# Kernel optimization log

Measured on AMD Instinct MI355X. Metric: run time of the kernel, lower is better.

## Reference

```python
import jax, jax.numpy as jnp
import numpy as np

N, B, D_IN, UNITS, K = 8192, 1, 2, 64, 2
F = D_IN + UNITS        # concatenated feature size per node
M = K + 1               # number of diffusion matrices (x0..xK)


def setup_inputs() -> dict:
    key = jax.random.key(0)
    k1, k2, k3, k4, k5, k6 = jax.random.split(key, 6)
    inputs = jax.random.normal(k1, (B, N * D_IN), dtype=jnp.float32)
    hx = jax.random.normal(k2, (B, N * UNITS), dtype=jnp.float32)
    adj = jax.random.uniform(k3, (N, N), dtype=jnp.float32)
    w_ru = jax.random.normal(k4, (F * M, 2 * UNITS), dtype=jnp.float32) * (2.0 / (F * M + 2 * UNITS)) ** 0.5
    b_ru = jnp.ones((2 * UNITS,), dtype=jnp.float32)  # bias_start=1.0 for gates
    w_c = jax.random.normal(k5, (F * M, UNITS), dtype=jnp.float32) * (2.0 / (F * M + UNITS)) ** 0.5
    b_c = jnp.zeros((UNITS,), dtype=jnp.float32)
    node_index = jax.random.randint(k6, (N,), 0, N)
    return {"inputs": inputs, "hx": hx, "adj": adj, "w_ru": w_ru,
            "b_ru": b_ru, "w_c": w_c, "b_c": b_c, "node_index": node_index}


def _gconv(adj_mx, inp, state, W, b, out_size):
    # inp: [B, N, D_IN], state: [B, N, UNITS]
    x = jnp.concatenate([inp, state], axis=2)              # [B, N, F]
    x0 = jnp.transpose(x, (1, 2, 0)).reshape(N, F * B)     # [N, F*B]
    xs = [x0]
    x1 = adj_mx @ x0                                       # 1-hop diffusion
    xs.append(x1)
    for _ in range(2, K + 1):                              # Chebyshev-style recurrence
        x2 = 2.0 * (adj_mx @ x1) - x0
        xs.append(x2)
        x0, x1 = x1, x2
    xk = jnp.stack(xs, 0).reshape(M, N, F, B)              # [M, N, F, B]
    xk = jnp.transpose(xk, (3, 1, 2, 0)).reshape(B * N, F * M)
    out = xk @ W + b                                       # [B*N, out_size]
    return out.reshape(B, N * out_size)


def reference(inputs, hx, adj, w_ru, b_ru, w_c, b_c, node_index):
    # square adj branch: adj_mx = ((D^-1)(A+I))^T, d_mat_inv = I (unused)
    adj2 = adj + jnp.eye(N, dtype=adj.dtype)
    d_inv = 1.0 / jnp.sum(adj2, axis=1)                    # no inf: diagonal added
    adj_mx = (adj2 * d_inv[:, None]).T
    inp = inputs.reshape(B, N, D_IN)
    h3 = hx.reshape(B, N, UNITS)
    value = jax.nn.sigmoid(_gconv(adj_mx, inp, h3, w_ru, b_ru, 2 * UNITS))
    value = value.reshape(B, N, 2 * UNITS)
    r = value[..., :UNITS].reshape(B, N * UNITS)
    u = value[..., UNITS:].reshape(B, N * UNITS)
    c = jnp.tanh(_gconv(adj_mx, inp, (r * hx).reshape(B, N, UNITS), w_c, b_c, UNITS))
    new_state = u * hx + (1.0 - u) * c                     # [B, N*UNITS]
    return new_state
```

## Files before the change

### kernel.cpp

```cpp
#include <hip/hip_runtime.h>
#include <math.h>


typedef __attribute__((ext_vector_type(4))) float f32x4;
typedef __attribute__((ext_vector_type(2))) int v2i;
typedef __attribute__((ext_vector_type(4))) int v4i;
typedef unsigned char uch;

constexpr int NN  = 8192;
constexpr int CST = 80;
constexpr int KBT = 256;
constexpr int SFT = KBT / 2;
constexpr int MCH = 4;
constexpr size_t NS    = (size_t)NN * CST;
constexpr size_t UTFS8 = (size_t)SFT * 5 * 1024;

constexpr float SC1  = 4096.f,   ISC1 = 1.f / 4096.f;
constexpr float SC2  = 262144.f, ISC2 = 1.f / 262144.f;

static __device__ __forceinline__ unsigned f2e4m3(float x) {
  union { float f; unsigned u; } c; c.f = x;
  unsigned s = (c.u >> 24) & 0x80u;
  float a = fabsf(x);
  if (a >= 464.f) return s | 0x7Eu;
  if (a < 0.015625f) {
    int q = (int)(a * 512.f + 0.5f);
    return s | (unsigned)q;
  }
  c.f = a;
  unsigned u = c.u + (0x7FFFFu + ((c.u >> 20) & 1u));
  int e = (int)((u >> 23) & 0xFFu) - 127;
  unsigned m = (u >> 20) & 7u;
  if (e > 8) return s | 0x7Eu;
  return s | (unsigned)(((e + 7) << 3) | m);
}

static __device__ __forceinline__ void mfma_f8(f32x4& acc, v2i a, v2i b) {
  asm("v_mfma_f32_16x16x32_fp8_fp8 %0, %1, %2, %0" : "+v"(acc) : "v"(a), "v"(b));
}
static __device__ __forceinline__ v2i lo2(v4i v) { v2i r; r.x = v.x; r.y = v.y; return r; }
static __device__ __forceinline__ v2i hi2(v4i v) { v2i r; r.x = v.z; r.y = v.w; return r; }

__global__ __launch_bounds__(256, 4) void k_conv(const float* __restrict__ adj,
                                                 uch* __restrict__ adjF8,
                                                 float* __restrict__ dpart) {
  __shared__ float tile[2][32][132];
  const int kb = blockIdx.x, mc = blockIdx.y;
  const int tid = threadIdx.x;
  const int l = tid & 63, w = tid >> 6;
  const int rg = tid >> 5;
  const int cb = (tid & 31) * 4;
  const float* src = adj + ((size_t)kb * 32 + rg) * NN + (size_t)mc * 2048 + cb;
  float rs[4] = {0.f, 0.f, 0.f, 0.f};
  float4 vA[4], vB[4];

#pragma unroll
  for (int i = 0; i < 4; ++i)
    vA[i] = *(const float4*)(src + (size_t)(8 * i) * NN);

#define CONV_BODY(CH, BUF, VC, VN)                                             \
  {                                                                            \
    const int ch_ = (CH);                                                      \
    _Pragma("unroll") for (int i = 0; i < 4; ++i) {                            \
      int r = rg + 8 * i;                                                      \
      int colp = (cb + 8 * i) & 127;                                           \
      *(float4*)&tile[BUF][r][colp] = VC[i];                                   \
      rs[i] += (VC[i].x + VC[i].y) + (VC[i].z + VC[i].w);                      \
    }                                                                          \
    if (ch_ < 15) {                                                            \
      _Pragma("unroll") for (int i = 0; i < 4; ++i)                            \
          VN[i] = *(const float4*)(src + (size_t)(8 * i) * NN + (ch_ + 1) * 128); \
    }                                                                          \
    __syncthreads();                                                           \
    _Pragma("unroll") for (int h = 0; h < 2; ++h) {                            \
      int fl = w + 4 * h;                                                      \
      int mt = mc * 128 + ch_ * 8 + fl;                                        \
      int colp = (fl * 16 + (l & 15) + 8 * (l >> 4)) & 127;                    \
      unsigned plo = 0, phi = 0;                                               \
      _Pragma("unroll") for (int j = 0; j < 4; ++j)                            \
        plo |= f2e4m3(tile[BUF][8 * (l >> 4) + j][colp]) << (8 * j);           \
      _Pragma("unroll") for (int j = 4; j < 8; ++j)                            \
        phi |= f2e4m3(tile[BUF][8 * (l >> 4) + j][colp]) << (8 * (j - 4));     \
      uint2 pk; pk.x = plo; pk.y = phi;                                        \
      *(uint2*)(adjF8 + ((size_t)mt * SFT + (kb >> 1)) * 1024                  \
                + l * 16 + (kb & 1) * 8) = pk;                                 \
    }                                                                          \
  }

  for (int cp = 0; cp < 8; ++cp) {
    CONV_BODY(2 * cp,     0, vA, vB);
    CONV_BODY(2 * cp + 1, 1, vB, vA);
  }
#undef CONV_BODY

#pragma unroll
  for (int i = 0; i < 4; ++i) {
#pragma unroll
    for (int m = 16; m >= 1; m >>= 1) rs[i] += __shfl_xor(rs[i], m);
  }
  if ((tid & 31) == 0) {
#pragma unroll
    for (int i = 0; i < 4; ++i)
      dpart[(size_t)mc * NN + kb * 32 + 8 * i + rg] = rs[i];
  }
}

__global__ __launch_bounds__(256) void k_build(const float* __restrict__ hx,
                                               const float* __restrict__ inp,
                                               const float* __restrict__ dpart,
                                               float* __restrict__ dinv,
                                               float* __restrict__ X0,
                                               float* __restrict__ XS0,
                                               uch* __restrict__ UtF8) {
  __shared__ float dv_s[32];
  const int bid = blockIdx.x;
  const int n0 = bid * 32;
  const int tid = threadIdx.x;
  if (tid < 32) {
    int n = n0 + tid;
    float dv = 1.f / (dpart[n] + dpart[NN + n] + dpart[2 * NN + n] +
                      dpart[3 * NN + n] + 1.f);
    dv_s[tid] = dv;
    dinv[n] = dv;
  }
  __syncthreads();
  for (int p = tid; p < 32 * 20; p += 256) {
    int nl = p / 20, c4 = (p % 20) * 4;
    int n = n0 + nl;
    float dv = dv_s[nl];
    float v[4];
#pragma unroll
    for (int j = 0; j < 4; ++j) {
      int c = c4 + j;
      v[j] = (c < 64) ? hx[n * 64 + c] : (c < 66 ? inp[n * 2 + (c - 64)] : 0.f);
    }
    size_t o = (size_t)n * CST + c4;
    *(float4*)(X0 + o)  = make_float4(v[0], v[1], v[2], v[3]);
    *(float4*)(XS0 + o) = make_float4(dv * v[0], dv * v[1], dv * v[2], dv * v[3]);
  }
  for (int p = tid; p < 5 * 64; p += 256) {
    int nt = p >> 6, l = p & 63;
    unsigned plo = 0, phi = 0;
#pragma unroll
    for (int j = 0; j < 8; ++j) {
      int nloc = 8 * (l >> 4) + j;
      int n = n0 + nloc;
      int c = nt * 16 + (l & 15);
      float v = (c < 64) ? hx[n * 64 + c] : (c < 66 ? inp[n * 2 + (c - 64)] : 0.f);
      unsigned b = f2e4m3(v * dv_s[nloc] * SC1);
      if (j < 4) plo |= b << (8 * j); else phi |= b << (8 * (j - 4));
    }
    uint2 pk; pk.x = plo; pk.y = phi;
    *(uint2*)(UtF8 + ((size_t)(bid >> 1) * 5 + nt) * 1024 + l * 16 + (bid & 1) * 8) = pk;
  }
}

static __device__ __forceinline__ void gemm_core2(const uch* __restrict__ adjF8,
                                                  const uch* __restrict__ bF8,
                                                  int bid, int tid, float* smem,
                                                  float sv[5], float inv_scale) {
  const int w8 = tid >> 6, l = tid & 63;
  const int sf0 = w8 * 16;
  f32x4 acc0[5], acc1[5];
#pragma unroll
  for (int nt = 0; nt < 5; ++nt) {
    acc0[nt] = (f32x4){0.f, 0.f, 0.f, 0.f};
    acc1[nt] = (f32x4){0.f, 0.f, 0.f, 0.f};
  }
  const uch* ap = adjF8 + ((size_t)(2 * bid) * SFT + sf0) * 1024 + l * 16;
  const size_t MSTR = (size_t)SFT * 1024;
  const uch* bp = bF8 + (size_t)sf0 * 5 * 1024 + l * 16;

  v4i A0e, A1e, A0o, A1o, Be[5], Bo[5];
  A0e = *(const v4i*)(ap);
  A1e = *(const v4i*)(ap + MSTR);
#pragma unroll
  for (int nt = 0; nt < 5; ++nt) Be[nt] = *(const v4i*)(bp + nt * 1024);

  for (int sf = 0; sf < 16; sf += 2) {
    A0o = *(const v4i*)(ap + (size_t)(sf + 1) * 1024);
    A1o = *(const v4i*)(ap + MSTR + (size_t)(sf + 1) * 1024);
#pragma unroll
    for (int nt = 0; nt < 5; ++nt)
      Bo[nt] = *(const v4i*)(bp + (size_t)((sf + 1) * 5 + nt) * 1024);
#pragma unroll
    for (int nt = 0; nt < 5; ++nt) {
      mfma_f8(acc0[nt], lo2(A0e), lo2(Be[nt]));
      mfma_f8(acc1[nt], lo2(A1e), lo2(Be[nt]));
    }
#pragma unroll
    for (int nt = 0; nt < 5; ++nt) {
      mfma_f8(acc0[nt], hi2(A0e), hi2(Be[nt]));
      mfma_f8(acc1[nt], hi2(A1e), hi2(Be[nt]));
    }
    A0e = *(const v4i*)(ap + (size_t)(sf + 2) * 1024);
    A1e = *(const v4i*)(ap + MSTR + (size_t)(sf + 2) * 1024);
#pragma unroll
    for (int nt = 0; nt < 5; ++nt)
      Be[nt] = *(const v4i*)(bp + (size_t)((sf + 2) * 5 + nt) * 1024);
#pragma unroll
    for (int nt = 0; nt < 5; ++nt) {
      mfma_f8(acc0[nt], lo2(A0o), lo2(Bo[nt]));
      mfma_f8(acc1[nt], lo2(A1o), lo2(Bo[nt]));
    }
#pragma unroll
    for (int nt = 0; nt < 5; ++nt) {
      mfma_f8(acc0[nt], hi2(A0o), hi2(Bo[nt]));
      mfma_f8(acc1[nt], hi2(A1o), hi2(Bo[nt]));
    }
  }
  asm volatile("s_nop 7\n\ts_nop 7\n\ts_nop 7" ::: "memory");

  auto red = reinterpret_cast<float(*)[64][40]>(smem);
  if (w8 < 4) {
#pragma unroll
    for (int nt = 0; nt < 5; ++nt) {
      *(f32x4*)&red[w8][l][nt * 4]      = acc0[nt];
      *(f32x4*)&red[w8][l][20 + nt * 4] = acc1[nt];
    }
  }
  __syncthreads();
  if (w8 >= 4) {
#pragma unroll
    for (int nt = 0; nt < 5; ++nt) {
      f32x4 t0 = *(f32x4*)&red[w8 - 4][l][nt * 4];
      f32x4 t1 = *(f32x4*)&red[w8 - 4][l][20 + nt * 4];
      *(f32x4*)&red[w8 - 4][l][nt * 4]      = t0 + acc0[nt];
      *(f32x4*)&red[w8 - 4][l][20 + nt * 4] = t1 + acc1[nt];
    }
  }
  __syncthreads();
#pragma unroll
  for (int i = 0; i < 5; ++i) {
    int p = tid + i * 512;
    int r = p / 80, c = p % 80;
    int mtl = r >> 4, rl = r & 15;
    int ll = ((rl >> 2) << 4) | (c & 15);
    int slot = mtl * 20 + (((c >> 4) << 2) | (rl & 3));
    sv[i] = (((red[0][ll][slot] + red[1][ll][slot]) +
              red[2][ll][slot]) + red[3][ll][slot]) * inv_scale;
  }
  __syncthreads();
}

__global__ __launch_bounds__(512, 1) void k_hop1(const uch* __restrict__ adjF8,
                                                 const uch* __restrict__ UtFin,
                                                 const float* __restrict__ XSin,
                                                 const float* __restrict__ dinv,
                                                 float* __restrict__ X1,
                                                 float* __restrict__ XS1,
                                                 uch* __restrict__ UtFout) {
  __shared__ __align__(16) float smem[10240];
  const int bid = blockIdx.x, tid = threadIdx.x;
  const int n0 = bid * 32;
  float sv[5];
  gemm_core2(adjF8, UtFin, bid, tid, smem, sv, ISC1);

  auto xs = reinterpret_cast<float(*)[80]>(smem);
#pragma unroll
  for (int i = 0; i < 5; ++i) {
    int p = tid + i * 512;
    size_t o = (size_t)n0 * CST + p;
    float x1 = XSin[o] + sv[i];
    X1[o] = x1;
    float z = dinv[n0 + p / 80] * x1;
    XS1[o] = z;
    xs[p / 80][p % 80] = z;
  }
  __syncthreads();
  for (int p = tid; p < 5 * 64; p += 512) {
    int nt = p >> 6, l = p & 63;
    unsigned plo = 0, phi = 0;
#pragma unroll
    for (int j = 0; j < 8; ++j) {
      unsigned b = f2e4m3(xs[8 * (l >> 4) + j][nt * 16 + (l & 15)] * SC2);
      if (j < 4) plo |= b << (8 * j); else phi |= b << (8 * (j - 4));
    }
    uint2 pk; pk.x = plo; pk.y = phi;
    *(uint2*)(UtFout + ((size_t)(bid >> 1) * 5 + nt) * 1024 + l * 16 + (bid & 1) * 8) = pk;
  }
}

__global__ __launch_bounds__(512, 1) void k_hop2g(const uch* __restrict__ adjF8,
    const uch* __restrict__ UtFb, const float* __restrict__ XS1,
    const float* __restrict__ X0, const float* __restrict__ X1,
    const float* __restrict__ w_ru, const float* __restrict__ b_ru,
    const float* __restrict__ hx, const float* __restrict__ inp,
    const float* __restrict__ dinv,
    float* __restrict__ X0w, float* __restrict__ XS0w,
    uch* __restrict__ UtFa, float* __restrict__ UG) {
  __shared__ __align__(16) float smem[10240];
  const int bid = blockIdx.x, tid = threadIdx.x;
  const int n0 = bid * 32;
  float sv[5];
  gemm_core2(adjF8, UtFb, bid, tid, smem, sv, ISC2);

  auto xr2 = reinterpret_cast<float(*)[80]>(smem);
  float* xr01 = smem + 2560;
  float* rhq  = smem + 2560 + 4352;
#pragma unroll
  for (int i = 0; i < 5; ++i) {
    int p = tid + i * 512;
    size_t o = (size_t)n0 * CST + p;
    xr2[p / 80][p % 80] = 2.f * (XS1[o] + sv[i]) - X0[o];
  }
  for (int p = tid; p < 32 * 17; p += 512) {
    int nl = p / 17, c4 = (p % 17) * 4;
    size_t o = (size_t)(n0 + nl) * CST + c4;
    *(float4*)&xr01[nl * 68 + c4]            = *(const float4*)(X0 + o);
    *(float4*)&xr01[32 * 68 + nl * 68 + c4]  = *(const float4*)(X1 + o);
  }
  __syncthreads();

  const int nl = tid >> 4, og = tid & 15, o0 = og * 8;
  float acc[8];
#pragma unroll
  for (int j = 0; j < 8; ++j) acc[j] = b_ru[o0 + j];
  for (int c = 0; c < 66; ++c) {
    int f = (c < 64) ? (c + 2) : (c - 64);
    const float* wr = w_ru + (size_t)(f * 3) * 128 + o0;
    float xv[3];
    xv[0] = xr01[nl * 68 + c];
    xv[1] = xr01[32 * 68 + nl * 68 + c];
    xv[2] = xr2[nl][c];
#pragma unroll
    for (int m = 0; m < 3; ++m) {
      float wl[8];
      *(float4*)(wl)     = *(const float4*)(wr + m * 128);
      *(float4*)(wl + 4) = *(const float4*)(wr + m * 128 + 4);
#pragma unroll
      for (int j = 0; j < 8; ++j) acc[j] += xv[m] * wl[j];
    }
  }
  const int n = n0 + nl;
  const float dv = dinv[n];
  if (og < 8) {
#pragma unroll
    for (int j = 0; j < 8; ++j) {
      int o = o0 + j;
      float r = 1.f / (1.f + expf(-acc[j]));
      float rh = r * hx[n * 64 + o];
      X0w[(size_t)n * CST + o] = rh;
      float srh = dv * rh;
      XS0w[(size_t)n * CST + o] = srh;
      rhq[nl * 64 + o] = srh;
    }
  } else {
#pragma unroll
    for (int j = 0; j < 8; ++j)
      UG[n * 64 + (o0 - 64) + j] = 1.f / (1.f + expf(-acc[j]));
  }
  __syncthreads();
  for (int p = tid; p < 5 * 64; p += 512) {
    int nt = p >> 6, l = p & 63;
    unsigned plo = 0, phi = 0;
#pragma unroll
    for (int j = 0; j < 8; ++j) {
      int lr = 8 * (l >> 4) + j;
      int nn = n0 + lr;
      int c = nt * 16 + (l & 15);
      float v;
      if (c < 64)      v = rhq[lr * 64 + c];
      else if (c < 66) v = dinv[nn] * inp[nn * 2 + (c - 64)];
      else             v = 0.f;
      unsigned b = f2e4m3(v * SC1);
      if (j < 4) plo |= b << (8 * j); else phi |= b << (8 * (j - 4));
    }
    uint2 pk; pk.x = plo; pk.y = phi;
    *(uint2*)(UtFa + ((size_t)(bid >> 1) * 5 + nt) * 1024 + l * 16 + (bid & 1) * 8) = pk;
  }
}

__global__ __launch_bounds__(512, 1) void k_hop2f(const uch* __restrict__ adjF8,
    const uch* __restrict__ UtFb, const float* __restrict__ XS1,
    const float* __restrict__ X0, const float* __restrict__ X1,
    const float* __restrict__ w_c, const float* __restrict__ b_c,
    const float* __restrict__ hx, const float* __restrict__ UG,
    float* __restrict__ out) {
  __shared__ __align__(16) float smem[10240];
  const int bid = blockIdx.x, tid = threadIdx.x;
  const int n0 = bid * 32;
  float sv[5];
  gemm_core2(adjF8, UtFb, bid, tid, smem, sv, ISC2);

  auto xr2 = reinterpret_cast<float(*)[80]>(smem);
  float* xr01 = smem + 2560;
#pragma unroll
  for (int i = 0; i < 5; ++i) {
    int p = tid + i * 512;
    size_t o = (size_t)n0 * CST + p;
    xr2[p / 80][p % 80] = 2.f * (XS1[o] + sv[i]) - X0[o];
  }
  for (int p = tid; p < 32 * 17; p += 512) {
    int nl = p / 17, c4 = (p % 17) * 4;
    size_t o = (size_t)(n0 + nl) * CST + c4;
    *(float4*)&xr01[nl * 68 + c4]           = *(const float4*)(X0 + o);
    *(float4*)&xr01[32 * 68 + nl * 68 + c4] = *(const float4*)(X1 + o);
  }
  __syncthreads();

  const int nl = tid >> 4, ot = tid & 15, o0 = ot * 4;
  float acc[4];
#pragma unroll
  for (int j = 0; j < 4; ++j) acc[j] = b_c[o0 + j];
  for (int c = 0; c < 66; ++c) {
    int f = (c < 64) ? (c + 2) : (c - 64);
    float xv[3];
    xv[0] = xr01[nl * 68 + c];
    xv[1] = xr01[32 * 68 + nl * 68 + c];
    xv[2] = xr2[nl][c];
#pragma unroll
    for (int m = 0; m < 3; ++m) {
      float wl[4];
      *(float4*)(wl) = *(const float4*)(w_c + (size_t)(f * 3 + m) * 64 + o0);
#pragma unroll
      for (int j = 0; j < 4; ++j) acc[j] += xv[m] * wl[j];
    }
  }
  const int n = n0 + nl;
#pragma unroll
  for (int j = 0; j < 4; ++j) {
    int o = o0 + j;
    float cc = tanhf(acc[j]);
    float u = UG[n * 64 + o];
    float h = hx[n * 64 + o];
    out[n * 64 + o] = u * h + (1.f - u) * cc;
  }
}

extern "C" void kernel_launch(void* const* d_in, const int* in_sizes, int n_in,
                              void* d_out, int out_size, void* d_ws, size_t ws_size,
                              hipStream_t stream) {
  const float* inp  = (const float*)d_in[0];
  const float* hx   = (const float*)d_in[1];
  const float* adj  = (const float*)d_in[2];
  const float* w_ru = (const float*)d_in[3];
  const float* b_ru = (const float*)d_in[4];
  const float* w_c  = (const float*)d_in[5];
  const float* b_c  = (const float*)d_in[6];
  float* out = (float*)d_out;

  float* ws    = (float*)d_ws;
  float* dinv  = ws;
  float* dpart = ws + 8192;
  float* X0    = ws + 8192 + 4 * 8192;
  float* XS0   = X0 + NS;
  float* X1    = XS0 + NS;
  float* XS1   = X1 + NS;
  uch* UtFa8   = (uch*)(XS1 + NS);
  uch* UtFb8   = UtFa8 + UTFS8;
  uch* adjF8   = UtFb8 + UTFS8;
  float* UG    = (float*)(adjF8 + (size_t)512 * SFT * 1024);

  dim3 cg(KBT, MCH);

  k_conv <<<cg, 256, 0, stream>>>(adj, adjF8, dpart);
  k_build<<<NN / 32, 256, 0, stream>>>(hx, inp, dpart, dinv, X0, XS0, UtFa8);

  k_hop1 <<<256, 512, 0, stream>>>(adjF8, UtFa8, XS0, dinv, X1, XS1, UtFb8);
  k_hop2g<<<256, 512, 0, stream>>>(adjF8, UtFb8, XS1, X0, X1, w_ru, b_ru, hx, inp,
                                   dinv, X0, XS0, UtFa8, UG);

  k_hop1 <<<256, 512, 0, stream>>>(adjF8, UtFa8, XS0, dinv, X1, XS1, UtFb8);
  k_hop2f<<<256, 512, 0, stream>>>(adjF8, UtFb8, XS1, X0, X1, w_c, b_c, hx, UG, out);
}
```

Before: 228.5 us.

## Halve per-block row tile to one 16-row M-tile, doubling grid to 512 blocks

The hop kernels now give each block a single 16-row M tile instead of two. The grid doubles from 256 to 512 blocks, shared memory is halved, and launch bounds allow several blocks per CU. The goal is to fill all CUs on MI355X (256 CUs) and improve latency hiding in these memory-bound fp8 GEMMs. The cost is that each B (UtF) fragment is loaded once per 16-row block rather than shared across two M tiles, which doubles B-operand traffic. The epilogue output tiling and the fp8 packing write were reworked to match the half-tile layout.

```diff
diff --git a/kernel.cpp b/kernel.cpp
--- a/kernel.cpp
+++ b/kernel.cpp
@@ -155,133 +155,122 @@
   }
 }
 
-static __device__ __forceinline__ void gemm_core2(const uch* __restrict__ adjF8,
+static __device__ __forceinline__ void gemm_core1(const uch* __restrict__ adjF8,
                                                   const uch* __restrict__ bF8,
-                                                  int bid, int tid, float* smem,
-                                                  float sv[5], float inv_scale) {
+                                                  int mt, int tid, float* smem,
+                                                  float& sv0, float& sv1,
+                                                  float& sv2, float inv_scale) {
   const int w8 = tid >> 6, l = tid & 63;
   const int sf0 = w8 * 16;
-  f32x4 acc0[5], acc1[5];
-#pragma unroll
-  for (int nt = 0; nt < 5; ++nt) {
-    acc0[nt] = (f32x4){0.f, 0.f, 0.f, 0.f};
-    acc1[nt] = (f32x4){0.f, 0.f, 0.f, 0.f};
-  }
-  const uch* ap = adjF8 + ((size_t)(2 * bid) * SFT + sf0) * 1024 + l * 16;
-  const size_t MSTR = (size_t)SFT * 1024;
+  f32x4 acc[5];
+#pragma unroll
+  for (int nt = 0; nt < 5; ++nt) acc[nt] = (f32x4){0.f, 0.f, 0.f, 0.f};
+  const uch* ap = adjF8 + ((size_t)mt * SFT + sf0) * 1024 + l * 16;
   const uch* bp = bF8 + (size_t)sf0 * 5 * 1024 + l * 16;
 
-  v4i A0e, A1e, A0o, A1o, Be[5], Bo[5];
-  A0e = *(const v4i*)(ap);
-  A1e = *(const v4i*)(ap + MSTR);
+  v4i Ae, Ao, Be[5], Bo[5];
+  Ae = *(const v4i*)(ap);
 #pragma unroll
   for (int nt = 0; nt < 5; ++nt) Be[nt] = *(const v4i*)(bp + nt * 1024);
 
   for (int sf = 0; sf < 16; sf += 2) {
-    A0o = *(const v4i*)(ap + (size_t)(sf + 1) * 1024);
-    A1o = *(const v4i*)(ap + MSTR + (size_t)(sf + 1) * 1024);
+    Ao = *(const v4i*)(ap + (size_t)(sf + 1) * 1024);
 #pragma unroll
     for (int nt = 0; nt < 5; ++nt)
       Bo[nt] = *(const v4i*)(bp + (size_t)((sf + 1) * 5 + nt) * 1024);
 #pragma unroll
-    for (int nt = 0; nt < 5; ++nt) {
-      mfma_f8(acc0[nt], lo2(A0e), lo2(Be[nt]));
-      mfma_f8(acc1[nt], lo2(A1e), lo2(Be[nt]));
-    }
-#pragma unroll
-    for (int nt = 0; nt < 5; ++nt) {
-      mfma_f8(acc0[nt], hi2(A0e), hi2(Be[nt]));
-      mfma_f8(acc1[nt], hi2(A1e), hi2(Be[nt]));
-    }
-    A0e = *(const v4i*)(ap + (size_t)(sf + 2) * 1024);
-    A1e = *(const v4i*)(ap + MSTR + (size_t)(sf + 2) * 1024);
+    for (int nt = 0; nt < 5; ++nt) mfma_f8(acc[nt], lo2(Ae), lo2(Be[nt]));
+#pragma unroll
+    for (int nt = 0; nt < 5; ++nt) mfma_f8(acc[nt], hi2(Ae), hi2(Be[nt]));
+    Ae = *(const v4i*)(ap + (size_t)(sf + 2) * 1024);
 #pragma unroll
     for (int nt = 0; nt < 5; ++nt)
       Be[nt] = *(const v4i*)(bp + (size_t)((sf + 2) * 5 + nt) * 1024);
 #pragma unroll
+    for (int nt = 0; nt < 5; ++nt) mfma_f8(acc[nt], lo2(Ao), lo2(Bo[nt]));
+#pragma unroll
+    for (int nt = 0; nt < 5; ++nt) mfma_f8(acc[nt], hi2(Ao), hi2(Bo[nt]));
+  }
+  asm volatile("s_nop 7\n\ts_nop 7\n\ts_nop 7" ::: "memory");
+
+  auto red = reinterpret_cast<float(*)[64][20]>(smem);
+  if (w8 < 4) {
+#pragma unroll
+    for (int nt = 0; nt < 5; ++nt) *(f32x4*)&red[w8][l][nt * 4] = acc[nt];
+  }
+  __syncthreads();
+  if (w8 >= 4) {
+#pragma unroll
     for (int nt = 0; nt < 5; ++nt) {
-      mfma_f8(acc0[nt], lo2(A0o), lo2(Bo[nt]));
-      mfma_f8(acc1[nt], lo2(A1o), lo2(Bo[nt]));
-    }
-#pragma unroll
-    for (int nt = 0; nt < 5; ++nt) {
-      mfma_f8(acc0[nt], hi2(A0o), hi2(Bo[nt]));
-      mfma_f8(acc1[nt], hi2(A1o), hi2(Bo[nt]));
-    }
-  }
-  asm volatile("s_nop 7\n\ts_nop 7\n\ts_nop 7" ::: "memory");
-
-  auto red = reinterpret_cast<float(*)[64][40]>(smem);
-  if (w8 < 4) {
-#pragma unroll
-    for (int nt = 0; nt < 5; ++nt) {
-      *(f32x4*)&red[w8][l][nt * 4]      = acc0[nt];
-      *(f32x4*)&red[w8][l][20 + nt * 4] = acc1[nt];
-    }
-  }
-  __syncthreads();
-  if (w8 >= 4) {
-#pragma unroll
-    for (int nt = 0; nt < 5; ++nt) {
-      f32x4 t0 = *(f32x4*)&red[w8 - 4][l][nt * 4];
-      f32x4 t1 = *(f32x4*)&red[w8 - 4][l][20 + nt * 4];
-      *(f32x4*)&red[w8 - 4][l][nt * 4]      = t0 + acc0[nt];
-      *(f32x4*)&red[w8 - 4][l][20 + nt * 4] = t1 + acc1[nt];
-    }
-  }
-  __syncthreads();
-#pragma unroll
-  for (int i = 0; i < 5; ++i) {
-    int p = tid + i * 512;
-    int r = p / 80, c = p % 80;
-    int mtl = r >> 4, rl = r & 15;
-    int ll = ((rl >> 2) << 4) | (c & 15);
-    int slot = mtl * 20 + (((c >> 4) << 2) | (rl & 3));
-    sv[i] = (((red[0][ll][slot] + red[1][ll][slot]) +
-              red[2][ll][slot]) + red[3][ll][slot]) * inv_scale;
-  }
-  __syncthreads();
-}
-
-__global__ __launch_bounds__(512, 1) void k_hop1(const uch* __restrict__ adjF8,
+      f32x4 t = *(f32x4*)&red[w8 - 4][l][nt * 4];
+      *(f32x4*)&red[w8 - 4][l][nt * 4] = t + acc[nt];
+    }
+  }
+  __syncthreads();
+#define GATHER(P)                                                              \
+  ({ int p_ = (P); int r_ = p_ / 80, c_ = p_ % 80;                             \
+     int ll_ = ((r_ >> 2) << 4) | (c_ & 15);                                   \
+     int k_ = ((c_ >> 4) << 2) | (r_ & 3);                                     \
+     (((red[0][ll_][k_] + red[1][ll_][k_]) + red[2][ll_][k_])                  \
+      + red[3][ll_][k_]) * inv_scale; })
+  sv0 = GATHER(tid);
+  sv1 = GATHER(tid + 512);
+  sv2 = (tid < 256) ? GATHER(tid + 1024) : 0.f;
+#undef GATHER
+  __syncthreads();
+}
+
+#define UTF_WRITE_HALF(DST, VALEXPR, SCALE)                                    \
+  {                                                                            \
+    const int sfK = mt >> 2;                                                   \
+    const int byteoff = ((mt >> 1) & 1) * 8;                                   \
+    const int lbase = (mt & 1) * 32;                                           \
+    for (int p = tid; p < 5 * 32; p += 512) {                                  \
+      int nt = p >> 5, idx = p & 31;                                           \
+      int l2 = lbase + idx;                                                    \
+      unsigned plo = 0, phi = 0;                                               \
+      _Pragma("unroll") for (int j = 0; j < 8; ++j) {                          \
+        int lr = 8 * (idx >> 4) + j;                                           \
+        int cc = nt * 16 + (idx & 15);                                         \
+        float v_ = (VALEXPR);                                                  \
+        unsigned b_ = f2e4m3(v_ * (SCALE));                                    \
+        if (j < 4) plo |= b_ << (8 * j); else phi |= b_ << (8 * (j - 4));      \
+      }                                                                        \
+      uint2 pk; pk.x = plo; pk.y = phi;                                       \
+      *(uint2*)((DST) + ((size_t)sfK * 5 + nt) * 1024 + l2 * 16 + byteoff) = pk; \
+    }                                                                          \
+  }
+
+__global__ __launch_bounds__(512, 4) void k_hop1(const uch* __restrict__ adjF8,
                                                  const uch* __restrict__ UtFin,
                                                  const float* __restrict__ XSin,
                                                  const float* __restrict__ dinv,
                                                  float* __restrict__ X1,
                                                  float* __restrict__ XS1,
                                                  uch* __restrict__ UtFout) {
-  __shared__ __align__(16) float smem[10240];
-  const int bid = blockIdx.x, tid = threadIdx.x;
-  const int n0 = bid * 32;
-  float sv[5];
-  gemm_core2(adjF8, UtFin, bid, tid, smem, sv, ISC1);
+  __shared__ __align__(16) float smem[5120];
+  const int mt = blockIdx.x, tid = threadIdx.x;
+  const int n0 = mt * 16;
+  float sv0, sv1, sv2;
+  gemm_core1(adjF8, UtFin, mt, tid, smem, sv0, sv1, sv2, ISC1);
 
   auto xs = reinterpret_cast<float(*)[80]>(smem);
-#pragma unroll
-  for (int i = 0; i < 5; ++i) {
-    int p = tid + i * 512;
-    size_t o = (size_t)n0 * CST + p;
-    float x1 = XSin[o] + sv[i];
-    X1[o] = x1;
-    float z = dinv[n0 + p / 80] * x1;
-    XS1[o] = z;
-    xs[p / 80][p % 80] = z;
-  }
-  __syncthreads();
-  for (int p = tid; p < 5 * 64; p += 512) {
-    int nt = p >> 6, l = p & 63;
-    unsigned plo = 0, phi = 0;
-#pragma unroll
-    for (int j = 0; j < 8; ++j) {
-      unsigned b = f2e4m3(xs[8 * (l >> 4) + j][nt * 16 + (l & 15)] * SC2);
-      if (j < 4) plo |= b << (8 * j); else phi |= b << (8 * (j - 4));
-    }
-    uint2 pk; pk.x = plo; pk.y = phi;
-    *(uint2*)(UtFout + ((size_t)(bid >> 1) * 5 + nt) * 1024 + l * 16 + (bid & 1) * 8) = pk;
-  }
-}
-
-__global__ __launch_bounds__(512, 1) void k_hop2g(const uch* __restrict__ adjF8,
+#define HOP1_ITEM(P, SV)                                                       \
+  { int p_ = (P); size_t o_ = (size_t)n0 * CST + p_;                           \
+    float x1_ = XSin[o_] + (SV);                                               \
+    X1[o_] = x1_;                                                              \
+    float z_ = dinv[n0 + p_ / 80] * x1_;                                       \
+    XS1[o_] = z_;                                                              \
+    xs[p_ / 80][p_ % 80] = z_; }
+  HOP1_ITEM(tid, sv0)
+  HOP1_ITEM(tid + 512, sv1)
+  if (tid < 256) HOP1_ITEM(tid + 1024, sv2)
+#undef HOP1_ITEM
+  __syncthreads();
+  UTF_WRITE_HALF(UtFout, xs[lr][cc], SC2)
+}
+
+__global__ __launch_bounds__(512, 4) void k_hop2g(const uch* __restrict__ adjF8,
     const uch* __restrict__ UtFb, const float* __restrict__ XS1,
     const float* __restrict__ X0, const float* __restrict__ X1,
     const float* __restrict__ w_ru, const float* __restrict__ b_ru,
@@ -289,54 +278,54 @@
     const float* __restrict__ dinv,
     float* __restrict__ X0w, float* __restrict__ XS0w,
     uch* __restrict__ UtFa, float* __restrict__ UG) {
-  __shared__ __align__(16) float smem[10240];
-  const int bid = blockIdx.x, tid = threadIdx.x;
-  const int n0 = bid * 32;
-  float sv[5];
-  gemm_core2(adjF8, UtFb, bid, tid, smem, sv, ISC2);
+  __shared__ __align__(16) float smem[5120];
+  const int mt = blockIdx.x, tid = threadIdx.x;
+  const int n0 = mt * 16;
+  float sv0, sv1, sv2;
+  gemm_core1(adjF8, UtFb, mt, tid, smem, sv0, sv1, sv2, ISC2);
 
   auto xr2 = reinterpret_cast<float(*)[80]>(smem);
-  float* xr01 = smem + 2560;
-  float* rhq  = smem + 2560 + 4352;
-#pragma unroll
-  for (int i = 0; i < 5; ++i) {
-    int p = tid + i * 512;
-    size_t o = (size_t)n0 * CST + p;
-    xr2[p / 80][p % 80] = 2.f * (XS1[o] + sv[i]) - X0[o];
-  }
-  for (int p = tid; p < 32 * 17; p += 512) {
+  float* xr01 = smem + 1280;
+  float* rhq  = smem + 1280 + 2176;
+#define X2_ITEM(P, SV)                                                         \
+  { int p_ = (P); size_t o_ = (size_t)n0 * CST + p_;                           \
+    xr2[p_ / 80][p_ % 80] = 2.f * (XS1[o_] + (SV)) - X0[o_]; }
+  X2_ITEM(tid, sv0)
+  X2_ITEM(tid + 512, sv1)
+  if (tid < 256) X2_ITEM(tid + 1024, sv2)
+#undef X2_ITEM
+  for (int p = tid; p < 16 * 17; p += 512) {
     int nl = p / 17, c4 = (p % 17) * 4;
     size_t o = (size_t)(n0 + nl) * CST + c4;
     *(float4*)&xr01[nl * 68 + c4]            = *(const float4*)(X0 + o);
-    *(float4*)&xr01[32 * 68 + nl * 68 + c4]  = *(const float4*)(X1 + o);
-  }
-  __syncthreads();
-
-  const int nl = tid >> 4, og = tid & 15, o0 = og * 8;
-  float acc[8];
-#pragma unroll
-  for (int j = 0; j < 8; ++j) acc[j] = b_ru[o0 + j];
+    *(float4*)&xr01[16 * 68 + nl * 68 + c4]  = *(const float4*)(X1 + o);
+  }
+  __syncthreads();
+
+  const int nl = tid >> 5, og = tid & 31, o0 = og * 4;
+  float acc[4];
+#pragma unroll
+  for (int j = 0; j < 4; ++j) acc[j] = b_ru[o0 + j];
   for (int c = 0; c < 66; ++c) {
     int f = (c < 64) ? (c + 2) : (c - 64);
     const float* wr = w_ru + (size_t)(f * 3) * 128 + o0;
     float xv[3];
     xv[0] = xr01[nl * 68 + c];
-    xv[1] = xr01[32 * 68 + nl * 68 + c];
+    xv[1] = xr01[16 * 68 + nl * 68 + c];
     xv[2] = xr2[nl][c];
 #pragma unroll
     for (int m = 0; m < 3; ++m) {
-      float wl[8];
-      *(float4*)(wl)     = *(const float4*)(wr + m * 128);
-      *(float4*)(wl + 4) = *(const float4*)(wr + m * 128 + 4);
-#pragma unroll
-      for (int j = 0; j < 8; ++j) acc[j] += xv[m] * wl[j];
+      float wl[4];
+      *(float4*)(wl) = *(const float4*)(wr + m * 128);
+#pragma unroll
+      for (int j = 0; j < 4; ++j) acc[j] += xv[m] * wl[j];
     }
   }
   const int n = n0 + nl;
   const float dv = dinv[n];
-  if (og < 8) {
-#pragma unroll
-    for (int j = 0; j < 8; ++j) {
+  if (og < 16) {
+#pragma unroll
+    for (int j = 0; j < 4; ++j) {
       int o = o0 + j;
       float r = 1.f / (1.f + expf(-acc[j]));
       float rh = r * hx[n * 64 + o];
@@ -347,79 +336,67 @@
     }
   } else {
 #pragma unroll
-    for (int j = 0; j < 8; ++j)
+    for (int j = 0; j < 4; ++j)
       UG[n * 64 + (o0 - 64) + j] = 1.f / (1.f + expf(-acc[j]));
   }
   __syncthreads();
-  for (int p = tid; p < 5 * 64; p += 512) {
-    int nt = p >> 6, l = p & 63;
-    unsigned plo = 0, phi = 0;
-#pragma unroll
-    for (int j = 0; j < 8; ++j) {
-      int lr = 8 * (l >> 4) + j;
-      int nn = n0 + lr;
-      int c = nt * 16 + (l & 15);
-      float v;
-      if (c < 64)      v = rhq[lr * 64 + c];
-      else if (c < 66) v = dinv[nn] * inp[nn * 2 + (c - 64)];
-      else             v = 0.f;
-      unsigned b = f2e4m3(v * SC1);
-      if (j < 4) plo |= b << (8 * j); else phi |= b << (8 * (j - 4));
-    }
-    uint2 pk; pk.x = plo; pk.y = phi;
-    *(uint2*)(UtFa + ((size_t)(bid >> 1) * 5 + nt) * 1024 + l * 16 + (bid & 1) * 8) = pk;
-  }
-}
-
-__global__ __launch_bounds__(512, 1) void k_hop2f(const uch* __restrict__ adjF8,
+  UTF_WRITE_HALF(UtFa,
+                 (cc < 64) ? rhq[lr * 64 + cc]
+                           : ((cc < 66) ? dinv[n0 + lr] * inp[(n0 + lr) * 2 + (cc - 64)]
+                                        : 0.f),
+                 SC1)
+}
+
+__global__ __launch_bounds__(512, 4) void k_hop2f(const uch* __restrict__ adjF8,
     const uch* __restrict__ UtFb, const float* __restrict__ XS1,
     const float* __restrict__ X0, const float* __restrict__ X1,
     const float* __restrict__ w_c, const float* __restrict__ b_c,
     const float* __restrict__ hx, const float* __restrict__ UG,
     float* __restrict__ out) {
-  __shared__ __align__(16) float smem[10240];
-  const int bid = blockIdx.x, tid = threadIdx.x;
-  const int n0 = bid * 32;
-  float sv[5];
-  gemm_core2(adjF8, UtFb, bid, tid, smem, sv, ISC2);
+  __shared__ __align__(16) float smem[5120];
+  const int mt = blockIdx.x, tid = threadIdx.x;
+  const int n0 = mt * 16;
+  float sv0, sv1, sv2;
+  gemm_core1(adjF8, UtFb, mt, tid, smem, sv0, sv1, sv2, ISC2);
 
   auto xr2 = reinterpret_cast<float(*)[80]>(smem);
-  float* xr01 = smem + 2560;
-#pragma unroll
-  for (int i = 0; i < 5; ++i) {
-    int p = tid + i * 512;
-    size_t o = (size_t)n0 * CST + p;
-    xr2[p / 80][p % 80] = 2.f * (XS1[o] + sv[i]) - X0[o];
-  }
-  for (int p = tid; p < 32 * 17; p += 512) {
+  float* xr01 = smem + 1280;
+#define X2_ITEM(P, SV)                                                         \
+  { int p_ = (P); size_t o_ = (size_t)n0 * CST + p_;                           \
+    xr2[p_ / 80][p_ % 80] = 2.f * (XS1[o_] + (SV)) - X0[o_]; }
+  X2_ITEM(tid, sv0)
+  X2_ITEM(tid + 512, sv1)
+  if (tid < 256) X2_ITEM(tid + 1024, sv2)
+#undef X2_ITEM
+  for (int p = tid; p < 16 * 17; p += 512) {
     int nl = p / 17, c4 = (p % 17) * 4;
     size_t o = (size_t)(n0 + nl) * CST + c4;
     *(float4*)&xr01[nl * 68 + c4]           = *(const float4*)(X0 + o);
-    *(float4*)&xr01[32 * 68 + nl * 68 + c4] = *(const float4*)(X1 + o);
-  }
-  __syncthreads();
-
-  const int nl = tid >> 4, ot = tid & 15, o0 = ot * 4;
-  float acc[4];
-#pragma unroll
-  for (int j = 0; j < 4; ++j) acc[j] = b_c[o0 + j];
+    *(float4*)&xr01[16 * 68 + nl * 68 + c4] = *(const float4*)(X1 + o);
+  }
+  __syncthreads();
+
+  const int nl = tid >> 5, ot = tid & 31, o0 = ot * 2;
+  float acc[2];
+#pragma unroll
+  for (int j = 0; j < 2; ++j) acc[j] = b_c[o0 + j];
   for (int c = 0; c < 66; ++c) {
     int f = (c < 64) ? (c + 2) : (c - 64);
     float xv[3];
     xv[0] = xr01[nl * 68 + c];
-    xv[1] = xr01[32 * 68 + nl * 68 + c];
+    xv[1] = xr01[16 * 68 + nl * 68 + c];
     xv[2] = xr2[nl][c];
 #pragma unroll
     for (int m = 0; m < 3; ++m) {
-      float wl[4];
-      *(float4*)(wl) = *(const float4*)(w_c + (size_t)(f * 3 + m) * 64 + o0);
-#pragma unroll
-      for (int j = 0; j < 4; ++j) acc[j] += xv[m] * wl[j];
+      float wl[2];
+      *(float2*)(wl) = *(const float2*)(w_c + (size_t)(f * 3 + m) * 64 + o0);
+#pragma unroll
+      for (int j = 0; j < 2; ++j) acc[j] += xv[m] * wl[j];
     }
   }
   const int n = n0 + nl;
 #pragma unroll
-  for (int j = 0; j < 4; ++j) {
+  for (int j = 0; j < 2; ++j) {
     int o = o0 + j;
     float cc = tanhf(acc[j]);
     float u = UG[n * 64 + o];
@@ -457,10 +434,10 @@
   k_conv <<<cg, 256, 0, stream>>>(adj, adjF8, dpart);
   k_build<<<NN / 32, 256, 0, stream>>>(hx, inp, dpart, dinv, X0, XS0, UtFa8);
 
-  k_hop1 <<<256, 512, 0, stream>>>(adjF8, UtFa8, XS0, dinv, X1, XS1, UtFb8);
-  k_hop2g<<<256, 512, 0, stream>>>(adjF8, UtFb8, XS1, X0, X1, w_ru, b_ru, hx, inp,
+  k_hop1 <<<512, 512, 0, stream>>>(adjF8, UtFa8, XS0, dinv, X1, XS1, UtFb8);
+  k_hop2g<<<512, 512, 0, stream>>>(adjF8, UtFb8, XS1, X0, X1, w_ru, b_ru, hx, inp,
                                    dinv, X0, XS0, UtFa8, UG);
 
-  k_hop1 <<<256, 512, 0, stream>>>(adjF8, UtFa8, XS0, dinv, X1, XS1, UtFb8);
-  k_hop2f<<<256, 512, 0, stream>>>(adjF8, UtFb8, XS1, X0, X1, w_c, b_c, hx, UG, out);
-}
+  k_hop1 <<<512, 512, 0, stream>>>(adjF8, UtFa8, XS0, dinv, X1, XS1, UtFb8);
+  k_hop2f<<<512, 512, 0, stream>>>(adjF8, UtFb8, XS1, X0, X1, w_c, b_c, hx, UG, out);
+}
```

After: 229.2 us. About the same (+0.3%).
